# Optimization experiments

Hardware: AMD Instinct MI355X
Metric: run time of the kernel (lower is better)

Reference implementation:

```python
import jax, jax.numpy as jnp
import numpy as np

B, T, N, F, H = 64, 50, 24, 256, 256  # batch, timesteps, graph nodes, input feat, hidden


def setup_inputs() -> dict:
    key = jax.random.key(0)
    ks = jax.random.split(key, 12)
    sF = 1.0 / np.sqrt(F)
    sH = 1.0 / np.sqrt(H)
    u = lambda k, shape, s: jax.random.uniform(k, shape, jnp.float32, -s, s)
    return {
        "x": jax.random.normal(ks[0], (B, T, N, F), jnp.float32),
        "G": jax.random.normal(ks[1], (N, N), jnp.float32) / np.sqrt(N),
        "W_ih": u(ks[2], (4 * H, F), sF),
        "b_ih": u(ks[3], (4 * H,), sF),
        "W_hh": u(ks[4], (4 * H, H), sH),
        "b_hh": u(ks[5], (4 * H,), sH),
        "W_h1": u(ks[6], (H, F), sF),
        "b_h1": u(ks[7], (H,), sF),
        "W_h2": u(ks[8], (H, F), sF),
        "b_h2": u(ks[9], (H,), sF),
        "W_fc": u(ks[10], (H, H), sH),
        "b_fc": u(ks[11], (H,), sH),
    }


def graph_linear(G, x, W, b):
    # GraphLinear: node-mixing G then feature projection W, bias after mixing
    # x: [B, N, f_in] -> [B, N, f_out]
    return jnp.einsum('nm,bmf->bnf', G, x @ W.T) + b


def reference(x, G, W_ih, b_ih, W_hh, b_hh, W_h1, b_h1, W_h2, b_h2, W_fc, b_fc):
    x0 = x[:, 0]                                   # [B, N, F]
    h = graph_linear(G, x0, W_h1, b_h1)            # initial hidden
    c = graph_linear(G, x0, W_h2, b_h2)            # initial cell

    def step(carry, xt):
        h, c = carry
        gates = (graph_linear(G, xt, W_ih, b_ih)
                 + graph_linear(G, h, W_hh, b_hh))  # [B, N, 4H]
        i, f, g, o = jnp.split(gates, 4, axis=-1)
        c = jax.nn.sigmoid(f) * c + jax.nn.sigmoid(i) * jnp.tanh(g)
        h = jax.nn.sigmoid(o) * jnp.tanh(c)
        return (h, c), None

    (h, c), _ = jax.lax.scan(step, (h, c), jnp.swapaxes(x, 0, 1))  # scan over T
    # dropout(p=0.0) is identity; final projection + tanh on last timestep output
    return jnp.tanh(graph_linear(G, h, W_fc, b_fc))
```

## Files before the change

kernel.cpp:

```cpp
#include <hip/hip_runtime.h>
#include <stdint.h>

#define T_ 50

typedef float f32x4 __attribute__((ext_vector_type(4)));
typedef short s16x8 __attribute__((ext_vector_type(8)));

#define WS_WIH   0u
#define WS_WHH   524288u
#define WS_WINIT 1048576u
#define WS_WFC   1310720u
#define WS_GPAD  1441792u
#define WS_FLG   1443840u
#define WS_NEED  1460224u

#define L_WHH 0
#define L_A1  131072
#define L_A2  143360
#define L_ZR  155648
#define L_HST 156160
#define L_TOT 161280

__device__ __forceinline__ uint32_t bfbits(float f){
  uint32_t u = __builtin_bit_cast(uint32_t, f);
  u += 0x7FFFu + ((u >> 16) & 1u);
  return u >> 16;
}
__device__ __forceinline__ uint32_t pk2bf(float lo, float hi){
  return bfbits(lo) | (bfbits(hi) << 16);
}
__device__ __forceinline__ f32x4 mfma16(s16x8 a, s16x8 b, f32x4 c){
  return __builtin_amdgcn_mfma_f32_16x16x32_bf16(a, b, c, 0, 0, 0);
}
#define LOG2E 1.4426950408889634f
__device__ __forceinline__ float fexp2(float x){ return __builtin_amdgcn_exp2f(x); }
__device__ __forceinline__ float frcp_(float x){ return __builtin_amdgcn_rcpf(x); }
__device__ __forceinline__ float fsig(float x){ return frcp_(1.f + fexp2(-LOG2E * x)); }
__device__ __forceinline__ float ftanh_(float x){ return 1.f - 2.f * frcp_(1.f + fexp2(2.f * LOG2E * x)); }

__global__ void prep_kernel(const float* __restrict__ G,
                            const float* __restrict__ Wih, const float* __restrict__ Whh,
                            const float* __restrict__ Wh1, const float* __restrict__ Wh2,
                            const float* __restrict__ Wfc, uint8_t* __restrict__ ws)
{
  const int tid = blockIdx.x * blockDim.x + threadIdx.x;
  const int nth = gridDim.x * blockDim.x;
  uint16_t* wih = (uint16_t*)(ws + WS_WIH);
  uint16_t* whh = (uint16_t*)(ws + WS_WHH);
  uint16_t* wini= (uint16_t*)(ws + WS_WINIT);
  uint16_t* wfc = (uint16_t*)(ws + WS_WFC);
  uint16_t* gp  = (uint16_t*)(ws + WS_GPAD);
  uint32_t* flg = (uint32_t*)(ws + WS_FLG);

  for (int i = tid; i < 262144; i += nth){
    int cg = i >> 16, c = (i >> 8) & 255, k = i & 255;
    int row = (c >> 6)*256 + 64*cg + (c & 63);
    wih[i] = (uint16_t)bfbits(Wih[row*256 + k]);
    whh[i] = (uint16_t)bfbits(Whh[row*256 + k]);
  }
  for (int i = tid; i < 131072; i += nth){
    int cg = i >> 15, c = (i >> 8) & 127, k = i & 255;
    float v = (c < 64) ? Wh1[(64*cg + c)*256 + k] : Wh2[(64*cg + c - 64)*256 + k];
    wini[i] = (uint16_t)bfbits(v);
  }
  for (int i = tid; i < 65536; i += nth){
    int cg = i >> 14, c = (i >> 8) & 63, k = i & 255;
    wfc[i] = (uint16_t)bfbits(Wfc[(64*cg + c)*256 + k]);
  }
  for (int i = tid; i < 1024; i += nth){
    int n = i >> 5, m = i & 31;
    gp[i] = (n < 24 && m < 24) ? (uint16_t)bfbits(G[n*24 + m]) : (uint16_t)0;
  }
  for (int i = tid; i < 4096; i += nth) flg[i] = 0;
}

__global__ void __launch_bounds__(512, 1)
encoder_kernel(const float* __restrict__ x, uint8_t* __restrict__ ws,
               float* __restrict__ out,
               const float* __restrict__ bih, const float* __restrict__ bhh,
               const float* __restrict__ bh1, const float* __restrict__ bh2,
               const float* __restrict__ bfc)
{
  extern __shared__ uint8_t smem[];
  uint16_t* WHHL = (uint16_t*)(smem + L_WHH);
  uint16_t* A1   = (uint16_t*)(smem + L_A1);
  uint16_t* A2   = (uint16_t*)(smem + L_A2);
  uint16_t* ZR   = (uint16_t*)(smem + L_ZR);
  uint16_t* HST  = (uint16_t*)(smem + L_HST);

  const int tid = threadIdx.x;
  const int b   = blockIdx.x & 63;
  const int cg  = blockIdx.x >> 6;
  const int w   = tid >> 6;
  const int l   = tid & 63;
  const int l15 = l & 15;
  const int g   = l >> 4;
  const int Mt  = w >> 2;
  const int ns  = w & 3;
  const int ul  = ns*16 + l15;
  const int ug  = 64*cg + ul;

  const uint16_t* WIH  = (const uint16_t*)(ws + WS_WIH)   + (size_t)cg*65536;
  const uint16_t* WINI = (const uint16_t*)(ws + WS_WINIT) + (size_t)cg*32768;
  const uint16_t* WFC  = (const uint16_t*)(ws + WS_WFC)   + (size_t)cg*16384;
  const uint16_t* GP   = (const uint16_t*)(ws + WS_GPAD);
  uint32_t* flg   = (uint32_t*)(ws + WS_FLG) + b*64;
  uint32_t* myflg = flg + cg*16;
  uint16_t* GhB = (uint16_t*)((uint8_t*)out + (size_t)b*24576);

  {
    const uint8_t* src = ws + WS_WHH + (size_t)cg*131072;
    for (int i = tid*8; i < 65536; i += 4096){
      uint4 v = *(const uint4*)(src + (size_t)i*2);
      int col = i >> 8, k0 = i & 255;
      *(uint4*)&WHHL[col*256 + (k0 ^ ((col&7)<<3))] = v;
    }
  }
  for (int i = tid; i < 256;  i += 512) ZR[i] = 0;
  for (int i = tid; i < 2560; i += 512) HST[i] = 0;

  s16x8 gfrag = *(const s16x8*)&GP[(Mt*16 + l15)*32 + g*8];

  const float bb0 = bih[ug]     + bhh[ug];
  const float bb1 = bih[256+ug] + bhh[256+ug];
  const float bb2 = bih[512+ug] + bhh[512+ug];
  const float bb3 = bih[768+ug] + bhh[768+ug];
  const float bh1l = bh1[ug], bh2l = bh2[ug], bfcl = bfc[ug];

  const int arow = Mt*16 + l15;
  const int sw   = (arow < 24) ? ((arow & 7) << 3) : 0;
  const uint16_t* a1row = (arow < 24) ? (A1 + arow*256) : ZR;
  const uint16_t* a2row = (arow < 24) ? (A2 + arow*256) : ZR;

  auto gx_stage = [&](const float* xt){
    #pragma unroll
    for (int jt = 0; jt < 4; jt++){
      int f = (jt*4 + ns)*16 + l15;
      s16x8 bfrag;
      if (g < 3){
        uint32_t p0 = pk2bf(xt[(g*8+0)*256+f], xt[(g*8+1)*256+f]);
        uint32_t p1 = pk2bf(xt[(g*8+2)*256+f], xt[(g*8+3)*256+f]);
        uint32_t p2 = pk2bf(xt[(g*8+4)*256+f], xt[(g*8+5)*256+f]);
        uint32_t p3 = pk2bf(xt[(g*8+6)*256+f], xt[(g*8+7)*256+f]);
        uint4 q; q.x = p0; q.y = p1; q.z = p2; q.w = p3;
        bfrag = __builtin_bit_cast(s16x8, q);
      } else {
        bfrag = (s16x8){0,0,0,0,0,0,0,0};
      }
      f32x4 zz = {0.f,0.f,0.f,0.f};
      f32x4 gx = mfma16(gfrag, bfrag, zz);
      #pragma unroll
      for (int r = 0; r < 4; r++){
        int node = Mt*16 + g*4 + r;
        if (node < 24) A2[node*256 + (f ^ ((node&7)<<3))] = (uint16_t)bfbits(gx[r]);
      }
    }
  };

  auto buildA1 = [&](int parity){
    const unsigned long long* gsrc = (const unsigned long long*)(GhB + parity*6144);
    for (int w_ = tid; w_ < 1536; w_ += 512){
      unsigned long long v = __hip_atomic_load((unsigned long long*)(gsrc + w_),
                              __ATOMIC_RELAXED, __HIP_MEMORY_SCOPE_AGENT);
      int cgs  = w_ / 384;
      int rem  = w_ - cgs*384;
      int unit = rem / 6;
      int node0= (rem - unit*6)*4;
      int k    = cgs*64 + unit;
      #pragma unroll
      for (int j = 0; j < 4; j++){
        int node = node0 + j;
        A1[node*256 + (k ^ ((node&7)<<3))] = (uint16_t)(v >> (16*j));
      }
    }
  };

  auto publish = [&](int parity, uint32_t flagval){
    s16x8 hb = *(const s16x8*)&HST[ul*40 + g*8];
    f32x4 zz = {0.f,0.f,0.f,0.f};
    f32x4 gh = mfma16(gfrag, hb, zz);
    int node0 = Mt*16 + g*4;
    if (node0 < 24){
      unsigned long long pv = (unsigned long long)pk2bf(gh[0], gh[1])
                            | ((unsigned long long)pk2bf(gh[2], gh[3]) << 32);
      unsigned long long* gd = (unsigned long long*)(GhB + parity*6144);
      __hip_atomic_store(gd + (cg*1536 + ul*24 + node0)/4, pv,
                         __ATOMIC_RELAXED, __HIP_MEMORY_SCOPE_AGENT);
    }
    asm volatile("s_waitcnt vmcnt(0)" ::: "memory");
    __syncthreads();
    if (tid == 0)
      __hip_atomic_store(myflg, flagval, __ATOMIC_RELAXED, __HIP_MEMORY_SCOPE_AGENT);
  };

  auto wait_for = [&](uint32_t target){
    if (tid < 4){
      uint32_t* fp = flg + tid*16;
      int guard = 0;
      while (__hip_atomic_load(fp, __ATOMIC_RELAXED, __HIP_MEMORY_SCOPE_AGENT) < target){
        __builtin_amdgcn_s_sleep(1);
        if (++guard > 50000000) break;
      }
    }
    __syncthreads();
  };

  float cst[4];
  f32x4 zacc[4];

  gx_stage(x + (size_t)b*T_*6144);
  __syncthreads();
  {
    f32x4 h0a = {0.f,0.f,0.f,0.f}, c0a = {0.f,0.f,0.f,0.f};
    #pragma unroll
    for (int j = 0; j < 4; j++) zacc[j] = (f32x4){0.f,0.f,0.f,0.f};
    #pragma unroll
    for (int ks = 0; ks < 8; ks++){
      s16x8 a  = *(const s16x8*)&a2row[(ks*32 + g*8) ^ sw];
      s16x8 b1 = *(const s16x8*)&WINI[ul*256 + ks*32 + g*8];
      s16x8 b2 = *(const s16x8*)&WINI[(64+ul)*256 + ks*32 + g*8];
      h0a = mfma16(a, b1, h0a);
      c0a = mfma16(a, b2, c0a);
      #pragma unroll
      for (int j = 0; j < 4; j++){
        s16x8 bz = *(const s16x8*)&WIH[((j*4+ns)*16 + l15)*256 + ks*32 + g*8];
        zacc[j] = mfma16(a, bz, zacc[j]);
      }
    }
    #pragma unroll
    for (int r = 0; r < 4; r++){
      cst[r] = c0a[r] + bh2l;
      int node = Mt*16 + g*4 + r;
      if (node < 24) HST[ul*40 + node] = (uint16_t)bfbits(h0a[r] + bh1l);
    }
  }
  __syncthreads();
  publish(1, 1u);

  for (int t = 0; t < T_; t++){
    wait_for((uint32_t)(t+1));
    buildA1((t+1)&1);
    __syncthreads();

    f32x4 uacc[4];
    #pragma unroll
    for (int j = 0; j < 4; j++) uacc[j] = zacc[j];
    #pragma unroll
    for (int ks = 0; ks < 8; ks++){
      s16x8 a = *(const s16x8*)&a1row[(ks*32 + g*8) ^ sw];
      #pragma unroll
      for (int j = 0; j < 4; j++){
        int col = (j*4+ns)*16 + l15;
        s16x8 bf = *(const s16x8*)&WHHL[col*256 + ((ks*32 + g*8) ^ ((col&7)<<3))];
        uacc[j] = mfma16(a, bf, uacc[j]);
      }
    }
    #pragma unroll
    for (int r = 0; r < 4; r++){
      float ig = fsig  (uacc[0][r] + bb0);
      float fg = fsig  (uacc[1][r] + bb1);
      float gg = ftanh_(uacc[2][r] + bb2);
      float og = fsig  (uacc[3][r] + bb3);
      float c  = fg*cst[r] + ig*gg;
      cst[r] = c;
      float h = og*ftanh_(c);
      int node = Mt*16 + g*4 + r;
      if (node < 24) HST[ul*40 + node] = (uint16_t)bfbits(h);
    }
    __syncthreads();
    publish(t & 1, (uint32_t)(t+2));

    if (t+1 < T_){
      gx_stage(x + ((size_t)b*T_ + (t+1))*6144);
      __syncthreads();
      #pragma unroll
      for (int j = 0; j < 4; j++) zacc[j] = (f32x4){0.f,0.f,0.f,0.f};
      #pragma unroll
      for (int ks = 0; ks < 8; ks++){
        s16x8 a = *(const s16x8*)&a2row[(ks*32 + g*8) ^ sw];
        #pragma unroll
        for (int j = 0; j < 4; j++){
          s16x8 bf = *(const s16x8*)&WIH[((j*4+ns)*16 + l15)*256 + ks*32 + g*8];
          zacc[j] = mfma16(a, bf, zacc[j]);
        }
      }
    }
  }

  wait_for((uint32_t)(T_+1));
  buildA1(1);
  __syncthreads();
  if (tid == 0)
    __hip_atomic_store(myflg, (uint32_t)(T_+2), __ATOMIC_RELAXED, __HIP_MEMORY_SCOPE_AGENT);
  wait_for((uint32_t)(T_+2));
  {
    f32x4 oacc = {0.f,0.f,0.f,0.f};
    #pragma unroll
    for (int ks = 0; ks < 8; ks++){
      s16x8 a  = *(const s16x8*)&a1row[(ks*32 + g*8) ^ sw];
      s16x8 bf = *(const s16x8*)&WFC[ul*256 + ks*32 + g*8];
      oacc = mfma16(a, bf, oacc);
    }
    #pragma unroll
    for (int r = 0; r < 4; r++){
      int node = Mt*16 + g*4 + r;
      if (node < 24)
        out[(size_t)b*6144 + node*256 + ug] = ftanh_(oacc[r] + bfcl);
    }
  }
}

extern "C" void kernel_launch(void* const* d_in, const int* in_sizes, int n_in,
                              void* d_out, int out_size, void* d_ws, size_t ws_size,
                              hipStream_t stream)
{
  (void)in_sizes; (void)n_in; (void)out_size;
  if (ws_size < WS_NEED) return;

  const float* x   = (const float*)d_in[0];
  const float* G   = (const float*)d_in[1];
  const float* Wih = (const float*)d_in[2];
  const float* bih = (const float*)d_in[3];
  const float* Whh = (const float*)d_in[4];
  const float* bhh = (const float*)d_in[5];
  const float* Wh1 = (const float*)d_in[6];
  const float* bh1 = (const float*)d_in[7];
  const float* Wh2 = (const float*)d_in[8];
  const float* bh2 = (const float*)d_in[9];
  const float* Wfc = (const float*)d_in[10];
  const float* bfc = (const float*)d_in[11];
  uint8_t* ws = (uint8_t*)d_ws;
  float* outp = (float*)d_out;

  hipLaunchKernelGGL(prep_kernel, dim3(256), dim3(256), 0, stream,
                     G, Wih, Whh, Wh1, Wh2, Wfc, ws);

  hipFuncSetAttribute((const void*)encoder_kernel,
                      hipFuncAttributeMaxDynamicSharedMemorySize, L_TOT);
  void* args[] = {(void*)&x, (void*)&ws, (void*)&outp,
                  (void*)&bih, (void*)&bhh, (void*)&bh1, (void*)&bh2, (void*)&bfc};
  hipLaunchCooperativeKernel((const void*)encoder_kernel, dim3(256), dim3(512),
                             args, L_TOT, stream);
}
```

Baseline: 649.7 us.

## Prefetch next-step input mixing and switch hidden exchange to node-major layout

The input-side graph mixing (gx_stage) for a future timestep is now issued right after the current gates are published. This lets its global loads overlap the cross-block wait rather than sit on the critical path between publish and the next recurrence. The shared hidden-state exchange buffer is reorganized to node-major order, staged through a new LDS buffer. Each block therefore writes coalesced 8-byte chunks and readers fill A1 with three vector loads and 8-byte LDS stores instead of scattered 16-bit stores. The cost is extra barriers and LDS inside the publish path, plus a larger LDS footprint.

```diff
diff --git a/kernel.cpp b/kernel.cpp
--- a/kernel.cpp
+++ b/kernel.cpp
@@ -14,13 +14,17 @@
 #define WS_FLG   1443840u
 #define WS_NEED  1460224u
 
-#define L_WHH 0
-#define L_A1  131072
-#define L_A2  143360
-#define L_ZR  155648
-#define L_HST 156160
-#define L_TOT 161280
-
+#define L_WHH  0
+#define L_A1   131072
+#define L_A2   143360
+#define L_ZR   155648
+#define L_HST  156160
+#define L_HST2 160256
+#define L_TOT  163328
+
+__device__ __forceinline__ f32x4 mfma16(s16x8 a, s16x8 b, f32x4 c){
+  return __builtin_amdgcn_mfma_f32_16x16x32_bf16(a, b, c, 0, 0, 0);
+}
 __device__ __forceinline__ uint32_t bfbits(float f){
   uint32_t u = __builtin_bit_cast(uint32_t, f);
   u += 0x7FFFu + ((u >> 16) & 1u);
@@ -28,9 +32,6 @@
 }
 __device__ __forceinline__ uint32_t pk2bf(float lo, float hi){
   return bfbits(lo) | (bfbits(hi) << 16);
-}
-__device__ __forceinline__ f32x4 mfma16(s16x8 a, s16x8 b, f32x4 c){
-  return __builtin_amdgcn_mfma_f32_16x16x32_bf16(a, b, c, 0, 0, 0);
 }
 #define LOG2E 1.4426950408889634f
 __device__ __forceinline__ float fexp2(float x){ return __builtin_amdgcn_exp2f(x); }
@@ -87,6 +88,7 @@
   uint16_t* A2   = (uint16_t*)(smem + L_A2);
   uint16_t* ZR   = (uint16_t*)(smem + L_ZR);
   uint16_t* HST  = (uint16_t*)(smem + L_HST);
+  uint16_t* HST2 = (uint16_t*)(smem + L_HST2);
 
   const int tid = threadIdx.x;
   const int b   = blockIdx.x & 63;
@@ -104,9 +106,9 @@
   const uint16_t* WINI = (const uint16_t*)(ws + WS_WINIT) + (size_t)cg*32768;
   const uint16_t* WFC  = (const uint16_t*)(ws + WS_WFC)   + (size_t)cg*16384;
   const uint16_t* GP   = (const uint16_t*)(ws + WS_GPAD);
-  uint32_t* flg   = (uint32_t*)(ws + WS_FLG) + b*64;
-  uint32_t* myflg = flg + cg*16;
-  uint16_t* GhB = (uint16_t*)((uint8_t*)out + (size_t)b*24576);
+  uint32_t* flgB = (uint32_t*)(ws + WS_FLG) + b*64;
+  uint32_t* flgW = flgB + cg*16;
+  uint16_t* GhB  = (uint16_t*)((uint8_t*)out + (size_t)b*24576);
 
   {
     const uint8_t* src = ws + WS_WHH + (size_t)cg*131072;
@@ -117,9 +119,9 @@
     }
   }
   for (int i = tid; i < 256;  i += 512) ZR[i] = 0;
-  for (int i = tid; i < 2560; i += 512) HST[i] = 0;
-
-  s16x8 gfrag = *(const s16x8*)&GP[(Mt*16 + l15)*32 + g*8];
+  for (int i = tid; i < 2048; i += 512) HST[i] = 0;
+
+  s16x8 gfragM = *(const s16x8*)&GP[(Mt*16 + l15)*32 + g*8];
 
   const float bb0 = bih[ug]     + bhh[ug];
   const float bb1 = bih[256+ug] + bhh[256+ug];
@@ -128,81 +130,88 @@
   const float bh1l = bh1[ug], bh2l = bh2[ug], bfcl = bfc[ug];
 
   const int arow = Mt*16 + l15;
-  const int sw   = (arow < 24) ? ((arow & 7) << 3) : 0;
   const uint16_t* a1row = (arow < 24) ? (A1 + arow*256) : ZR;
   const uint16_t* a2row = (arow < 24) ? (A2 + arow*256) : ZR;
+  const int sw = (arow < 24) ? ((arow & 7) << 3) : 0;
 
   auto gx_stage = [&](const float* xt){
     #pragma unroll
     for (int jt = 0; jt < 4; jt++){
       int f = (jt*4 + ns)*16 + l15;
-      s16x8 bfrag;
+      s16x8 bfrag = (s16x8){0,0,0,0,0,0,0,0};
       if (g < 3){
-        uint32_t p0 = pk2bf(xt[(g*8+0)*256+f], xt[(g*8+1)*256+f]);
-        uint32_t p1 = pk2bf(xt[(g*8+2)*256+f], xt[(g*8+3)*256+f]);
-        uint32_t p2 = pk2bf(xt[(g*8+4)*256+f], xt[(g*8+5)*256+f]);
-        uint32_t p3 = pk2bf(xt[(g*8+6)*256+f], xt[(g*8+7)*256+f]);
-        uint4 q; q.x = p0; q.y = p1; q.z = p2; q.w = p3;
+        uint4 q;
+        q.x = pk2bf(xt[(g*8+0)*256+f], xt[(g*8+1)*256+f]);
+        q.y = pk2bf(xt[(g*8+2)*256+f], xt[(g*8+3)*256+f]);
+        q.z = pk2bf(xt[(g*8+4)*256+f], xt[(g*8+5)*256+f]);
+        q.w = pk2bf(xt[(g*8+6)*256+f], xt[(g*8+7)*256+f]);
         bfrag = __builtin_bit_cast(s16x8, q);
-      } else {
-        bfrag = (s16x8){0,0,0,0,0,0,0,0};
       }
       f32x4 zz = {0.f,0.f,0.f,0.f};
-      f32x4 gx = mfma16(gfrag, bfrag, zz);
-      #pragma unroll
-      for (int r = 0; r < 4; r++){
-        int node = Mt*16 + g*4 + r;
-        if (node < 24) A2[node*256 + (f ^ ((node&7)<<3))] = (uint16_t)bfbits(gx[r]);
+      f32x4 gx = mfma16(gfragM, bfrag, zz);
+      int n0 = Mt*16 + g*4;
+      if (n0 < 24){
+        uint32_t a01 = pk2bf(gx[0], gx[1]), a23 = pk2bf(gx[2], gx[3]);
+        A2[(n0  )*256 + (f ^ (((n0  )&7)<<3))] = (uint16_t)a01;
+        A2[(n0+1)*256 + (f ^ (((n0+1)&7)<<3))] = (uint16_t)(a01>>16);
+        A2[(n0+2)*256 + (f ^ (((n0+2)&7)<<3))] = (uint16_t)a23;
+        A2[(n0+3)*256 + (f ^ (((n0+3)&7)<<3))] = (uint16_t)(a23>>16);
       }
     }
   };
 
-  auto buildA1 = [&](int parity){
-    const unsigned long long* gsrc = (const unsigned long long*)(GhB + parity*6144);
-    for (int w_ = tid; w_ < 1536; w_ += 512){
-      unsigned long long v = __hip_atomic_load((unsigned long long*)(gsrc + w_),
-                              __ATOMIC_RELAXED, __HIP_MEMORY_SCOPE_AGENT);
-      int cgs  = w_ / 384;
-      int rem  = w_ - cgs*384;
-      int unit = rem / 6;
-      int node0= (rem - unit*6)*4;
-      int k    = cgs*64 + unit;
-      #pragma unroll
-      for (int j = 0; j < 4; j++){
-        int node = node0 + j;
-        A1[node*256 + (k ^ ((node&7)<<3))] = (uint16_t)(v >> (16*j));
-      }
-    }
-  };
-
-  auto publish = [&](int parity, uint32_t flagval){
-    s16x8 hb = *(const s16x8*)&HST[ul*40 + g*8];
-    f32x4 zz = {0.f,0.f,0.f,0.f};
-    f32x4 gh = mfma16(gfrag, hb, zz);
-    int node0 = Mt*16 + g*4;
-    if (node0 < 24){
-      unsigned long long pv = (unsigned long long)pk2bf(gh[0], gh[1])
-                            | ((unsigned long long)pk2bf(gh[2], gh[3]) << 32);
-      unsigned long long* gd = (unsigned long long*)(GhB + parity*6144);
-      __hip_atomic_store(gd + (cg*1536 + ul*24 + node0)/4, pv,
-                         __ATOMIC_RELAXED, __HIP_MEMORY_SCOPE_AGENT);
-    }
-    asm volatile("s_waitcnt vmcnt(0)" ::: "memory");
-    __syncthreads();
-    if (tid == 0)
-      __hip_atomic_store(myflg, flagval, __ATOMIC_RELAXED, __HIP_MEMORY_SCOPE_AGENT);
+  auto stageA1 = [&](int parity){
+    const unsigned long long* gs = (const unsigned long long*)(GhB + parity*6144);
+    unsigned long long v0 = __hip_atomic_load(gs + tid,        __ATOMIC_RELAXED, __HIP_MEMORY_SCOPE_AGENT);
+    unsigned long long v1 = __hip_atomic_load(gs + tid + 512,  __ATOMIC_RELAXED, __HIP_MEMORY_SCOPE_AGENT);
+    unsigned long long v2 = __hip_atomic_load(gs + tid + 1024, __ATOMIC_RELAXED, __HIP_MEMORY_SCOPE_AGENT);
+    int k0 = (tid & 63) << 2;
+    int n0 = tid >> 6, n1 = n0 + 8, n2 = n0 + 16;
+    *(unsigned long long*)&A1[n0*256 + (k0 ^ ((n0&7)<<3))] = v0;
+    *(unsigned long long*)&A1[n1*256 + (k0 ^ ((n1&7)<<3))] = v1;
+    *(unsigned long long*)&A1[n2*256 + (k0 ^ ((n2&7)<<3))] = v2;
   };
 
   auto wait_for = [&](uint32_t target){
     if (tid < 4){
-      uint32_t* fp = flg + tid*16;
+      uint32_t* fp = flgB + tid*16;
       int guard = 0;
       while (__hip_atomic_load(fp, __ATOMIC_RELAXED, __HIP_MEMORY_SCOPE_AGENT) < target){
         __builtin_amdgcn_s_sleep(1);
-        if (++guard > 50000000) break;
-      }
-    }
-    __syncthreads();
+        if (++guard > 20000000) break;
+      }
+    }
+    __syncthreads();
+  };
+
+  auto do_publish = [&](const float hv[4], int parity, uint32_t flagval){
+    int n0 = Mt*16 + g*4;
+    if (n0 < 24){
+      uint2 p; p.x = pk2bf(hv[0], hv[1]); p.y = pk2bf(hv[2], hv[3]);
+      *(uint2*)&HST[ul*32 + n0] = p;
+    }
+    __syncthreads();
+    s16x8 hb = *(const s16x8*)&HST[ul*32 + g*8];
+    f32x4 zz = {0.f,0.f,0.f,0.f};
+    f32x4 gh = mfma16(gfragM, hb, zz);
+    if (n0 < 24){
+      uint32_t q01 = pk2bf(gh[0], gh[1]), q23 = pk2bf(gh[2], gh[3]);
+      HST2[(n0  )*64 + ul] = (uint16_t)q01;
+      HST2[(n0+1)*64 + ul] = (uint16_t)(q01>>16);
+      HST2[(n0+2)*64 + ul] = (uint16_t)q23;
+      HST2[(n0+3)*64 + ul] = (uint16_t)(q23>>16);
+    }
+    __syncthreads();
+    if (tid < 384){
+      int node = tid >> 4, c4 = tid & 15;
+      unsigned long long v = *(const unsigned long long*)&HST2[node*64 + c4*4];
+      __hip_atomic_store((unsigned long long*)(GhB + parity*6144) + node*64 + cg*16 + c4,
+                         v, __ATOMIC_RELAXED, __HIP_MEMORY_SCOPE_AGENT);
+    }
+    asm volatile("s_waitcnt vmcnt(0)" ::: "memory");
+    __syncthreads();
+    if (tid == 0)
+      __hip_atomic_store(flgW, flagval, __ATOMIC_RELAXED, __HIP_MEMORY_SCOPE_AGENT);
   };
 
   float cst[4];
@@ -216,30 +225,31 @@
     for (int j = 0; j < 4; j++) zacc[j] = (f32x4){0.f,0.f,0.f,0.f};
     #pragma unroll
     for (int ks = 0; ks < 8; ks++){
-      s16x8 a  = *(const s16x8*)&a2row[(ks*32 + g*8) ^ sw];
-      s16x8 b1 = *(const s16x8*)&WINI[ul*256 + ks*32 + g*8];
-      s16x8 b2 = *(const s16x8*)&WINI[(64+ul)*256 + ks*32 + g*8];
+      const int kk = ks*32 + g*8;
+      s16x8 a  = *(const s16x8*)&a2row[kk ^ sw];
+      s16x8 b1 = *(const s16x8*)&WINI[ul*256 + kk];
+      s16x8 b2 = *(const s16x8*)&WINI[(64+ul)*256 + kk];
       h0a = mfma16(a, b1, h0a);
       c0a = mfma16(a, b2, c0a);
       #pragma unroll
       for (int j = 0; j < 4; j++){
-        s16x8 bz = *(const s16x8*)&WIH[((j*4+ns)*16 + l15)*256 + ks*32 + g*8];
+        s16x8 bz = *(const s16x8*)&WIH[((j*4+ns)*16 + l15)*256 + kk];
         zacc[j] = mfma16(a, bz, zacc[j]);
       }
     }
+    float hv0[4];
     #pragma unroll
     for (int r = 0; r < 4; r++){
       cst[r] = c0a[r] + bh2l;
-      int node = Mt*16 + g*4 + r;
-      if (node < 24) HST[ul*40 + node] = (uint16_t)bfbits(h0a[r] + bh1l);
-    }
-  }
-  __syncthreads();
-  publish(1, 1u);
+      hv0[r] = h0a[r] + bh1l;
+    }
+    do_publish(hv0, 1, 1u);
+  }
+  gx_stage(x + ((size_t)b*T_ + 1)*6144);
 
   for (int t = 0; t < T_; t++){
     wait_for((uint32_t)(t+1));
-    buildA1((t+1)&1);
+    stageA1((t+1)&1);
     __syncthreads();
 
     f32x4 uacc[4];
@@ -247,14 +257,16 @@
     for (int j = 0; j < 4; j++) uacc[j] = zacc[j];
     #pragma unroll
     for (int ks = 0; ks < 8; ks++){
-      s16x8 a = *(const s16x8*)&a1row[(ks*32 + g*8) ^ sw];
+      const int kk = ks*32 + g*8;
+      s16x8 a = *(const s16x8*)&a1row[kk ^ sw];
       #pragma unroll
       for (int j = 0; j < 4; j++){
         int col = (j*4+ns)*16 + l15;
-        s16x8 bf = *(const s16x8*)&WHHL[col*256 + ((ks*32 + g*8) ^ ((col&7)<<3))];
+        s16x8 bf = *(const s16x8*)&WHHL[col*256 + (kk ^ ((col&7)<<3))];
         uacc[j] = mfma16(a, bf, uacc[j]);
       }
     }
+    float hv[4];
     #pragma unroll
     for (int r = 0; r < 4; r++){
       float ig = fsig  (uacc[0][r] + bb0);
@@ -263,49 +275,51 @@
       float og = fsig  (uacc[3][r] + bb3);
       float c  = fg*cst[r] + ig*gg;
       cst[r] = c;
-      float h = og*ftanh_(c);
-      int node = Mt*16 + g*4 + r;
-      if (node < 24) HST[ul*40 + node] = (uint16_t)bfbits(h);
-    }
-    __syncthreads();
-    publish(t & 1, (uint32_t)(t+2));
+      hv[r] = og*ftanh_(c);
+    }
+    do_publish(hv, t & 1, (uint32_t)(t+2));
 
     if (t+1 < T_){
-      gx_stage(x + ((size_t)b*T_ + (t+1))*6144);
-      __syncthreads();
       #pragma unroll
       for (int j = 0; j < 4; j++) zacc[j] = (f32x4){0.f,0.f,0.f,0.f};
       #pragma unroll
       for (int ks = 0; ks < 8; ks++){
-        s16x8 a = *(const s16x8*)&a2row[(ks*32 + g*8) ^ sw];
+        const int kk = ks*32 + g*8;
+        s16x8 a = *(const s16x8*)&a2row[kk ^ sw];
         #pragma unroll
         for (int j = 0; j < 4; j++){
-          s16x8 bf = *(const s16x8*)&WIH[((j*4+ns)*16 + l15)*256 + ks*32 + g*8];
+          s16x8 bf = *(const s16x8*)&WIH[((j*4+ns)*16 + l15)*256 + kk];
           zacc[j] = mfma16(a, bf, zacc[j]);
         }
       }
     }
+    __syncthreads();
+    if (t+1 < T_){
+      int tn = (t+2 < T_) ? (t+2) : (T_-1);
+      gx_stage(x + ((size_t)b*T_ + tn)*6144);
+    }
   }
 
   wait_for((uint32_t)(T_+1));
-  buildA1(1);
+  stageA1(1);
   __syncthreads();
   if (tid == 0)
-    __hip_atomic_store(myflg, (uint32_t)(T_+2), __ATOMIC_RELAXED, __HIP_MEMORY_SCOPE_AGENT);
+    __hip_atomic_store(flgW, (uint32_t)(T_+2), __ATOMIC_RELAXED, __HIP_MEMORY_SCOPE_AGENT);
   wait_for((uint32_t)(T_+2));
   {
     f32x4 oacc = {0.f,0.f,0.f,0.f};
     #pragma unroll
     for (int ks = 0; ks < 8; ks++){
-      s16x8 a  = *(const s16x8*)&a1row[(ks*32 + g*8) ^ sw];
-      s16x8 bf = *(const s16x8*)&WFC[ul*256 + ks*32 + g*8];
+      const int kk = ks*32 + g*8;
+      s16x8 a  = *(const s16x8*)&a1row[kk ^ sw];
+      s16x8 bf = *(const s16x8*)&WFC[ul*256 + kk];
       oacc = mfma16(a, bf, oacc);
     }
-    #pragma unroll
-    for (int r = 0; r < 4; r++){
-      int node = Mt*16 + g*4 + r;
-      if (node < 24)
-        out[(size_t)b*6144 + node*256 + ug] = ftanh_(oacc[r] + bfcl);
+    int n0 = Mt*16 + g*4;
+    if (n0 < 24){
+      #pragma unroll
+      for (int r = 0; r < 4; r++)
+        out[(size_t)b*6144 + (n0+r)*256 + ug] = ftanh_(oacc[r] + bfcl);
     }
   }
 }
```

Result: no change. 642.4 us (-1.1%).
